# Performance work log

Hardware: AMD Instinct MI355X
Metric: run time of the kernel (lower is better)

The kernel has to match this reference:

```python
import jax, jax.numpy as jnp
import numpy as np


def _hard_sigmoid(x):
    # Keras ConvLSTM2D default recurrent_activation
    return jnp.clip(0.2 * x + 0.5, 0.0, 1.0)


def _conv_same(x, w):
    # x: [B,H,W,Cin], w: [kh,kw,Cin,Cout]
    return jax.lax.conv_general_dilated(
        x, w, window_strides=(1, 1), padding='SAME',
        dimension_numbers=('NHWC', 'HWIO', 'NHWC'))


def setup_inputs() -> dict:
    key = jax.random.key(0)
    ks = jax.random.split(key, 6)
    B, T, H, W, F = 16, 16, 64, 64, 64
    return {
        'inputs': jax.random.normal(ks[0], (B, T, H, W, 1), jnp.float32),  # only T is used
        'h0': jax.random.normal(ks[1], (B, H, W, F), jnp.float32),
        'c0': jax.random.normal(ks[2], (B, H, W, F), jnp.float32),
        'kernels': jax.random.normal(ks[3], (T, 3, 3, F, 4 * F), jnp.float32) * 0.05,
        'rec_kernels': jax.random.normal(ks[4], (T, 3, 3, F, 4 * F), jnp.float32) * 0.05,
        'bias': jnp.zeros((T, 4 * F), jnp.float32),
    }


def reference(inputs, h0, c0, kernels, rec_kernels, bias):
    # The layer feeds h back as the cell input each step, so the cell input x == h.
    # By linearity, conv(h, Wk) + conv(h, Uk) == conv(h, Wk + Uk); we fuse the two convs.
    # Gate order (Keras ConvLSTM2DCell): i, f, c, o.
    def step(carry, params):
        h, c = carry
        Wk, Uk, b = params  # [3,3,F,4F], [3,3,F,4F], [4F]
        z = _conv_same(h, Wk + Uk) + b  # [B,H,W,4F]
        zi, zf, zc, zo = jnp.split(z, 4, axis=-1)
        i = _hard_sigmoid(zi)
        f = _hard_sigmoid(zf)
        c_new = f * c + i * jnp.tanh(zc)
        o = _hard_sigmoid(zo)
        h_new = o * jnp.tanh(c_new)
        return (h_new, c_new), h_new

    (_, _), hs = jax.lax.scan(step, (h0, c0), (kernels, rec_kernels, bias))
    return jnp.moveaxis(hs, 0, 1)  # [B, T, H, W, F]
```

## Files before the change

### kernel.cpp

```cpp
#include <hip/hip_runtime.h>
#include <math.h>

typedef _Float16 f16;
typedef _Float16 f16x4 __attribute__((ext_vector_type(4)));
typedef _Float16 f16x8 __attribute__((ext_vector_type(8)));
typedef float f32x4 __attribute__((ext_vector_type(4)));

#define NB 16
#define NT 16
#define NH 64
#define NW 64
#define NF 64
#define NG 256
#define HWF ((size_t)NH * NW * NF)
#define OUT_BSTRIDE ((size_t)NT * HWF)
#define RS2 8448
#define WSTEP ((size_t)18432)

#define MFMA(a, b, c) __builtin_amdgcn_mfma_f32_16x16x32_f16((a), (b), (c), 0, 0, 0)

__device__ __forceinline__ void gload_lds16(const void* g, void* l) {
    __builtin_amdgcn_global_load_lds(
        (const __attribute__((address_space(1))) unsigned int*)(g),
        (__attribute__((address_space(3))) unsigned int*)(l), 16, 0, 0);
}

__device__ __forceinline__ float hsig(float x) {
    return fminf(fmaxf(0.2f * x + 0.5f, 0.0f), 1.0f);
}

__device__ __forceinline__ float ftanh(float x) {
    float t = __builtin_amdgcn_exp2f(x * 2.885390081777927f);
    return 1.0f - 2.0f * __builtin_amdgcn_rcpf(t + 1.0f);
}

__global__ void fuse_w_hi(const float* __restrict__ k, const float* __restrict__ rk,
                          f16* __restrict__ wf2) {
    int idx = blockIdx.x * 256 + threadIdx.x;
    if (idx >= NT * 9 * NG * 8) return;
    int g8   = idx & 7;
    int cout = (idx >> 3) & 255;
    int tt   = idx >> 11;
    int tap  = tt % 9;
    int t    = tt / 9;
    int kk = g8 >> 2, lg = g8 & 3;

    const float* ks = k  + (size_t)tt * NF * NG + cout;
    const float* rs = rk + (size_t)tt * NF * NG + cout;

    f16 hi8[8];
#pragma unroll
    for (int j = 0; j < 8; ++j) {
        int cin = kk * 32 + lg * 8 + j;
        hi8[j] = (f16)(ks[(size_t)cin * NG] + rs[(size_t)cin * NG]);
    }
    const int lane = lg * 16 + (cout & 15);
    const int cb   = ((cout >> 4) & 3) * 4 + (cout >> 6);
    size_t chunk = (size_t)t * WSTEP + (size_t)(tap * 2 + kk) * 1024 +
                   (size_t)cb * 64 + lane;
    *(f16x8*)&wf2[chunk * 8] = *(f16x8*)hi8;
}

__global__ void f32_to_f16(const float* __restrict__ src, f16* __restrict__ dst, int n4) {
    int i = blockIdx.x * 256 + threadIdx.x;
    if (i >= n4) return;
    float4 v = ((const float4*)src)[i];
    f16x4 o = { (f16)v.x, (f16)v.y, (f16)v.z, (f16)v.w };
    *(f16x4*)&dst[(size_t)i * 4] = o;
}

__global__ void __launch_bounds__(512, 2)
convlstm_mfma_step(const f16* __restrict__ h2in, f16* __restrict__ h2out,
                   f16* __restrict__ cbuf,
                   float* __restrict__ hout,
                   const f16* __restrict__ wt,
                   const float* __restrict__ bias)
{
    __shared__ __align__(16) unsigned char lds[6 * RS2];

    const int tid  = threadIdx.x;
    const int w    = tid >> 6;
    const int lane = tid & 63;

    const int id = blockIdx.x;
    const int bb = ((id & 7) << 1) + ((id >> 7) & 1);
    const int y0 = ((id >> 3) & 15) * 4;

    const int wm = w >> 2;
    const int wn = w & 3;
    const int lm = lane & 15;
    const int lg = lane >> 4;

    const f16x8* wb = (const f16x8*)wt + (size_t)(wn * 4) * 64 + lane;
    f16x8 bh[4];
#pragma unroll
    for (int nf = 0; nf < 4; ++nf)
        bh[nf] = wb[nf * 64];

    const int f = wn * 16 + lm;
    f16 cp[8][4];
#pragma unroll
    for (int mf = 0; mf < 8; ++mf) {
        const int gy = y0 + wm * 2 + (mf >> 2);
        const int xb = (mf & 3) * 16 + lg * 4;
        const size_t base = ((((size_t)bb * NH + gy) * NW + xb) << 6) + f;
#pragma unroll
        for (int j = 0; j < 4; ++j)
            cp[mf][j] = cbuf[base + (size_t)j * 64];
    }

    if (tid < 96) {
        int row = tid >> 4, side = (tid >> 3) & 1, j = tid & 7;
        *(f16x8*)&lds[row * RS2 + side * (65 * 128) + j * 16] = (f16x8)(_Float16)0.0f;
    }

    {
        const int x = w * 8 + (lane >> 3);
        const int g = lane & 7;
        const unsigned src = ((unsigned)x << 7) +
                             ((unsigned)(g ^ ((x + 1) & 7)) << 4);
#pragma unroll
        for (int k = 0; k < 6; ++k) {
            const int gy = y0 - 1 + k;
            const unsigned dbase = k * RS2 + 128 + w * 1024;
            if (gy >= 0 && gy < NH) {
                const unsigned char* gsrc = (const unsigned char*)h2in +
                    ((((size_t)bb * NH + gy) * NW) << 7);
                gload_lds16(gsrc + src, (void*)&lds[dbase]);
            } else {
                *(f16x8*)&lds[dbase + lane * 16] = (f16x8)(_Float16)0.0f;
            }
        }
    }
    __syncthreads();

    f32x4 acc[8][4];
#pragma unroll
    for (int mf = 0; mf < 8; ++mf)
#pragma unroll
        for (int nf = 0; nf < 4; ++nf) acc[mf][nf] = (f32x4)0.0f;

    unsigned av[3][2];
#pragma unroll
    for (int d = 0; d < 3; ++d)
#pragma unroll
        for (int kk = 0; kk < 2; ++kk) {
            const int tx = lm + d;
            av[d][kk] = (unsigned)(tx * 128 +
                        (((kk * 4 + lg) ^ (tx & 7)) << 4));
        }

#pragma unroll
    for (int it = 0; it < 18; ++it) {
        if (it > 0) {
#pragma unroll
            for (int nf = 0; nf < 4; ++nf)
                bh[nf] = wb[(size_t)it * 1024 + nf * 64];
        }
        const int tap = it >> 1, kk = it & 1;
        const int ty = tap / 3;
        const int d  = tap - ty * 3;
        const unsigned abase = (unsigned)((wm * 2 + ty) * RS2) + av[d][kk];
        __builtin_amdgcn_s_setprio(1);
#pragma unroll
        for (int mf = 0; mf < 8; ++mf) {
            const f16x8 ah = *(const f16x8*)&lds[abase + (mf >> 2) * RS2 +
                                                 (mf & 3) * 2048];
#pragma unroll
            for (int nf = 0; nf < 4; ++nf)
                acc[mf][nf] = MFMA(ah, bh[nf], acc[mf][nf]);
        }
        __builtin_amdgcn_s_setprio(0);
    }

    const float b0 = bias[f], b1 = bias[64 + f], b2 = bias[128 + f], b3 = bias[192 + f];

#pragma unroll
    for (int mf = 0; mf < 8; ++mf) {
        const int gy = y0 + wm * 2 + (mf >> 2);
        const int xb = (mf & 3) * 16 + lg * 4;
        const size_t base = ((((size_t)bb * NH + gy) * NW + xb) << 6) + f;
#pragma unroll
        for (int j = 0; j < 4; ++j) {
            const float zi  = acc[mf][0][j] + b0;
            const float zfv = acc[mf][1][j] + b1;
            const float zc  = acc[mf][2][j] + b2;
            const float zo  = acc[mf][3][j] + b3;
            const float ig = hsig(zi), fg = hsig(zfv), og = hsig(zo);
            const float cn = fg * (float)cp[mf][j] + ig * ftanh(zc);
            cbuf[base + (size_t)j * 64] = (f16)cn;
            const float hn = og * ftanh(cn);
            hout[(size_t)bb * OUT_BSTRIDE + (((size_t)gy * NW + xb + j) << 6) + f] = hn;
            h2out[base + (size_t)j * 64] = (f16)hn;
        }
    }
}

extern "C" void kernel_launch(void* const* d_in, const int* in_sizes, int n_in,
                              void* d_out, int out_size, void* d_ws, size_t ws_size,
                              hipStream_t stream) {
    const float* h0    = (const float*)d_in[1];
    const float* c0    = (const float*)d_in[2];
    const float* kern  = (const float*)d_in[3];
    const float* rkern = (const float*)d_in[4];
    const float* bias  = (const float*)d_in[5];
    float* out = (float*)d_out;

    f16* wf2   = (f16*)d_ws;
    f16* h2a   = wf2 + (size_t)NT * WSTEP * 8;
    f16* h2b   = h2a + (size_t)NB * HWF;
    f16* cbuf  = h2b + (size_t)NB * HWF;

    const int n4 = (int)(NB * HWF / 4);
    fuse_w_hi<<<(NT * 9 * NG * 8 + 255) / 256, 256, 0, stream>>>(kern, rkern, wf2);
    f32_to_f16<<<(n4 + 255) / 256, 256, 0, stream>>>(h0, h2a, n4);
    f32_to_f16<<<(n4 + 255) / 256, 256, 0, stream>>>(c0, cbuf, n4);

    for (int t = 0; t < NT; ++t) {
        const f16* hin = (t & 1) ? h2b : h2a;
        f16* hnx       = (t & 1) ? h2a : h2b;
        convlstm_mfma_step<<<dim3(256), 512, 0, stream>>>(
            hin, hnx, cbuf,
            out + (size_t)t * HWF,
            wf2 + (size_t)t * WSTEP * 8,
            bias + t * NG);
    }
}
```

Before: 378.8 us.

## Fuse timestep launches into persistent cooperative kernel with neighbor flag sync

Replaces the 16 per-timestep launches with one cooperative persistent kernel. Each block keeps its h tile in LDS and its cell state in fp32 registers across steps, and exchanges only the halo rows with neighbouring y-blocks through global edge buffers and per-step flags. The aim is to remove launch overhead and the full reload of h and c every step. The cost is spin-wait synchronisation, system-scope stores and loads, and dependence on cooperative launch succeeding; the old multi-launch path stays as a fallback. The setprio hints are also dropped and the per-iteration weight load is moved up.

```diff
diff --git a/kernel.cpp b/kernel.cpp
--- a/kernel.cpp
+++ b/kernel.cpp
@@ -2,7 +2,7 @@
 #include <math.h>
 
 typedef _Float16 f16;
-typedef _Float16 f16x4 __attribute__((ext_vector_type(4)));
+typedef _Float16 f16x4v __attribute__((ext_vector_type(4)));
 typedef _Float16 f16x8 __attribute__((ext_vector_type(8)));
 typedef float f32x4 __attribute__((ext_vector_type(4)));
 
@@ -16,6 +16,7 @@
 #define OUT_BSTRIDE ((size_t)NT * HWF)
 #define RS2 8448
 #define WSTEP ((size_t)18432)
+#define FSTR 16
 
 #define MFMA(a, b, c) __builtin_amdgcn_mfma_f32_16x16x32_f16((a), (b), (c), 0, 0, 0)
 
@@ -65,16 +66,22 @@
     int i = blockIdx.x * 256 + threadIdx.x;
     if (i >= n4) return;
     float4 v = ((const float4*)src)[i];
-    f16x4 o = { (f16)v.x, (f16)v.y, (f16)v.z, (f16)v.w };
-    *(f16x4*)&dst[(size_t)i * 4] = o;
+    f16x4v o = { (f16)v.x, (f16)v.y, (f16)v.z, (f16)v.w };
+    *(f16x4v*)&dst[(size_t)i * 4] = o;
+}
+
+__global__ void zero_flags(int* __restrict__ flags) {
+    flags[blockIdx.x * 256 + threadIdx.x] = 0;
 }
 
 __global__ void __launch_bounds__(512, 2)
-convlstm_mfma_step(const f16* __restrict__ h2in, f16* __restrict__ h2out,
-                   f16* __restrict__ cbuf,
-                   float* __restrict__ hout,
-                   const f16* __restrict__ wt,
-                   const float* __restrict__ bias)
+convlstm_persist(const f16* __restrict__ wf2,
+                 const f16* __restrict__ h2init,
+                 f16* __restrict__ e0, f16* __restrict__ e1,
+                 const float* __restrict__ c0,
+                 float* __restrict__ out,
+                 const float* __restrict__ bias_all,
+                 int* __restrict__ flags)
 {
     __shared__ __align__(16) unsigned char lds[6 * RS2];
 
@@ -84,36 +91,209 @@
 
     const int id = blockIdx.x;
     const int bb = ((id & 7) << 1) + ((id >> 7) & 1);
-    const int y0 = ((id >> 3) & 15) * 4;
-
-    const int wm = w >> 2;
-    const int wn = w & 3;
-    const int lm = lane & 15;
-    const int lg = lane >> 4;
-
-    const f16x8* wb = (const f16x8*)wt + (size_t)(wn * 4) * 64 + lane;
-    f16x8 bh[4];
-#pragma unroll
-    for (int nf = 0; nf < 4; ++nf)
-        bh[nf] = wb[nf * 64];
-
-    const int f = wn * 16 + lm;
-    f16 cp[8][4];
+    const int iy = (id >> 3) & 15;
+    const int y0 = iy * 4;
+
+    const int wm = w >> 2, wn = w & 3, lm = lane & 15, lg = lane >> 4;
+    const int f  = wn * 16 + lm;
+
+    if (tid < 96) {
+        int row = tid >> 4, side = (tid >> 3) & 1, j = tid & 7;
+        *(f16x8*)&lds[row * RS2 + side * (65 * 128) + j * 16] = (f16x8)(_Float16)0.0f;
+    }
+    {
+        const int x = w * 8 + (lane >> 3);
+        const int g = lane & 7;
+        const unsigned src = ((unsigned)x << 7) +
+                             ((unsigned)(g ^ ((x + 1) & 7)) << 4);
+#pragma unroll
+        for (int k = 0; k < 6; ++k) {
+            const int gy = y0 - 1 + k;
+            const unsigned dbase = k * RS2 + 128 + w * 1024;
+            if (gy >= 0 && gy < NH) {
+                const unsigned char* gsrc = (const unsigned char*)h2init +
+                    ((((size_t)bb * NH + gy) * NW) << 7);
+                gload_lds16(gsrc + src, (void*)&lds[dbase]);
+            } else {
+                *(f16x8*)&lds[dbase + lane * 16] = (f16x8)(_Float16)0.0f;
+            }
+        }
+    }
+
+    float cp[8][4];
 #pragma unroll
     for (int mf = 0; mf < 8; ++mf) {
         const int gy = y0 + wm * 2 + (mf >> 2);
         const int xb = (mf & 3) * 16 + lg * 4;
         const size_t base = ((((size_t)bb * NH + gy) * NW + xb) << 6) + f;
 #pragma unroll
-        for (int j = 0; j < 4; ++j)
-            cp[mf][j] = cbuf[base + (size_t)j * 64];
+        for (int j = 0; j < 4; ++j) cp[mf][j] = c0[base + (size_t)j * 64];
+    }
+
+    unsigned av[3][2];
+#pragma unroll
+    for (int d = 0; d < 3; ++d)
+#pragma unroll
+        for (int kk = 0; kk < 2; ++kk) {
+            const int tx = lm + d;
+            av[d][kk] = (unsigned)(tx * 128 + (((kk * 4 + lg) ^ (tx & 7)) << 4));
+        }
+
+    __syncthreads();
+
+#pragma unroll 1
+    for (int t = 0; t < NT; ++t) {
+        const f16x8* wb = (const f16x8*)(wf2 + (size_t)t * WSTEP * 8) +
+                          (size_t)(wn * 4) * 64 + lane;
+        const float* bias = bias_all + t * NG;
+
+        f32x4 acc[8][4];
+#pragma unroll
+        for (int mf = 0; mf < 8; ++mf)
+#pragma unroll
+            for (int nf = 0; nf < 4; ++nf) acc[mf][nf] = (f32x4)0.0f;
+
+        f16x8 bh[4];
+#pragma unroll
+        for (int it = 0; it < 18; ++it) {
+#pragma unroll
+            for (int nf = 0; nf < 4; ++nf)
+                bh[nf] = wb[(size_t)it * 1024 + nf * 64];
+            const int tap = it >> 1, kk = it & 1;
+            const int ty = tap / 3;
+            const int d  = tap - ty * 3;
+            const unsigned abase = (unsigned)((wm * 2 + ty) * RS2) + av[d][kk];
+#pragma unroll
+            for (int mf = 0; mf < 8; ++mf) {
+                const f16x8 ah = *(const f16x8*)&lds[abase + (mf >> 2) * RS2 +
+                                                     (mf & 3) * 2048];
+#pragma unroll
+                for (int nf = 0; nf < 4; ++nf)
+                    acc[mf][nf] = MFMA(ah, bh[nf], acc[mf][nf]);
+            }
+        }
+
+        __syncthreads();
+
+        const float b0 = bias[f], b1 = bias[64 + f], b2 = bias[128 + f], b3 = bias[192 + f];
+        f16* eW = (t & 1) ? e1 : e0;
+        const bool last = (t == NT - 1);
+
+#pragma unroll
+        for (int mf = 0; mf < 8; ++mf) {
+            const int gy = y0 + wm * 2 + (mf >> 2);
+            const int xb = (mf & 3) * 16 + lg * 4;
+            const bool isEdge = (wm == 0) ? (mf < 4) : (mf >= 4);
+#pragma unroll
+            for (int j = 0; j < 4; ++j) {
+                const float zi  = acc[mf][0][j] + b0;
+                const float zfv = acc[mf][1][j] + b1;
+                const float zc  = acc[mf][2][j] + b2;
+                const float zo  = acc[mf][3][j] + b3;
+                const float ig = hsig(zi), fg = hsig(zfv), og = hsig(zo);
+                const float cn = fg * cp[mf][j] + ig * ftanh(zc);
+                cp[mf][j] = cn;
+                const float hn = og * ftanh(cn);
+                out[(size_t)bb * OUT_BSTRIDE + (size_t)t * HWF +
+                    (((size_t)gy * NW + xb + j) << 6) + f] = hn;
+                if (!last) {
+                    f16 hv = (f16)hn;
+                    const int x = xb + j;
+                    const unsigned loff = (unsigned)((wm * 2 + (mf >> 2) + 1) * RS2 +
+                        128 + x * 128 + (((f >> 3) ^ ((x + 1) & 7)) << 4) + (f & 7) * 2);
+                    *(f16*)&lds[loff] = hv;
+                    if (isEdge) {
+                        const f16* ep = eW + ((((size_t)bb * NH + gy) * NW + x) << 6) + f;
+                        int hb = (int)*(unsigned short*)&hv;
+                        asm volatile("global_store_short %0, %1, off sc0 sc1"
+                                     :: "v"(ep), "v"(hb) : "memory");
+                    }
+                }
+            }
+        }
+
+        if (!last) {
+            __syncthreads();
+
+            if (tid == 0) {
+                const int fbase = ((t * NB + bb) * 16) * FSTR;
+                __hip_atomic_store(&flags[fbase + iy * FSTR], 1,
+                                   __ATOMIC_RELAXED, __HIP_MEMORY_SCOPE_SYSTEM);
+                if (iy > 0)
+                    while (__hip_atomic_load(&flags[fbase + (iy - 1) * FSTR],
+                           __ATOMIC_RELAXED, __HIP_MEMORY_SCOPE_SYSTEM) == 0)
+                        __builtin_amdgcn_s_sleep(1);
+                if (iy < 15)
+                    while (__hip_atomic_load(&flags[fbase + (iy + 1) * FSTR],
+                           __ATOMIC_RELAXED, __HIP_MEMORY_SCOPE_SYSTEM) == 0)
+                        __builtin_amdgcn_s_sleep(1);
+            }
+            __syncthreads();
+
+            const int gi0 = tid * 2;
+            const int r   = gi0 >> 9;
+            const bool valid = r ? (iy < 15) : (iy > 0);
+            if (valid) {
+                const int gy = r ? (y0 + 4) : (y0 - 1);
+                const int rem0 = gi0 & 511, rem1 = rem0 + 1;
+                const int x0 = rem0 >> 3, g0 = rem0 & 7;
+                const int x1 = rem1 >> 3, g1 = rem1 & 7;
+                const f16* sp0 = eW + ((((size_t)bb * NH + gy) * NW + x0) << 6) + g0 * 8;
+                const f16* sp1 = eW + ((((size_t)bb * NH + gy) * NW + x1) << 6) + g1 * 8;
+                f16x8 v0, v1;
+                asm volatile("global_load_dwordx4 %0, %1, off sc0 sc1"
+                             : "=v"(v0) : "v"(sp0) : "memory");
+                asm volatile("global_load_dwordx4 %0, %1, off sc0 sc1"
+                             : "=v"(v1) : "v"(sp1) : "memory");
+                asm volatile("s_waitcnt vmcnt(0)" ::: "memory");
+                const unsigned slot = (r ? 5u : 0u) * RS2 + 128;
+                unsigned d0 = (unsigned)(uintptr_t)&lds[slot + x0 * 128 +
+                                                        ((g0 ^ ((x0 + 1) & 7)) << 4)];
+                unsigned d1 = (unsigned)(uintptr_t)&lds[slot + x1 * 128 +
+                                                        ((g1 ^ ((x1 + 1) & 7)) << 4)];
+                asm volatile("ds_write_b128 %0, %1" :: "v"(d0), "v"(v0) : "memory");
+                asm volatile("ds_write_b128 %0, %1" :: "v"(d1), "v"(v1) : "memory");
+            }
+            __syncthreads();
+        }
+    }
+}
+
+__global__ void __launch_bounds__(512, 2)
+convlstm_mfma_step(const f16* __restrict__ h2in, f16* __restrict__ h2out,
+                   f16* __restrict__ cbuf, float* __restrict__ hout,
+                   const f16* __restrict__ wt, const float* __restrict__ bias)
+{
+    __shared__ __align__(16) unsigned char lds[6 * RS2];
+
+    const int tid  = threadIdx.x;
+    const int w    = tid >> 6;
+    const int lane = tid & 63;
+    const int id = blockIdx.x;
+    const int bb = ((id & 7) << 1) + ((id >> 7) & 1);
+    const int y0 = ((id >> 3) & 15) * 4;
+    const int wm = w >> 2, wn = w & 3, lm = lane & 15, lg = lane >> 4;
+
+    const f16x8* wb = (const f16x8*)wt + (size_t)(wn * 4) * 64 + lane;
+    f16x8 bh[4];
+#pragma unroll
+    for (int nf = 0; nf < 4; ++nf) bh[nf] = wb[nf * 64];
+
+    const int f = wn * 16 + lm;
+    f16 cp[8][4];
+#pragma unroll
+    for (int mf = 0; mf < 8; ++mf) {
+        const int gy = y0 + wm * 2 + (mf >> 2);
+        const int xb = (mf & 3) * 16 + lg * 4;
+        const size_t base = ((((size_t)bb * NH + gy) * NW + xb) << 6) + f;
+#pragma unroll
+        for (int j = 0; j < 4; ++j) cp[mf][j] = cbuf[base + (size_t)j * 64];
     }
 
     if (tid < 96) {
         int row = tid >> 4, side = (tid >> 3) & 1, j = tid & 7;
         *(f16x8*)&lds[row * RS2 + side * (65 * 128) + j * 16] = (f16x8)(_Float16)0.0f;
     }
-
     {
         const int x = w * 8 + (lane >> 3);
         const int g = lane & 7;
@@ -146,8 +326,7 @@
 #pragma unroll
         for (int kk = 0; kk < 2; ++kk) {
             const int tx = lm + d;
-            av[d][kk] = (unsigned)(tx * 128 +
-                        (((kk * 4 + lg) ^ (tx & 7)) << 4));
+            av[d][kk] = (unsigned)(tx * 128 + (((kk * 4 + lg) ^ (tx & 7)) << 4));
         }
 
 #pragma unroll
@@ -161,7 +340,6 @@
         const int ty = tap / 3;
         const int d  = tap - ty * 3;
         const unsigned abase = (unsigned)((wm * 2 + ty) * RS2) + av[d][kk];
-        __builtin_amdgcn_s_setprio(1);
 #pragma unroll
         for (int mf = 0; mf < 8; ++mf) {
             const f16x8 ah = *(const f16x8*)&lds[abase + (mf >> 2) * RS2 +
@@ -170,11 +348,9 @@
             for (int nf = 0; nf < 4; ++nf)
                 acc[mf][nf] = MFMA(ah, bh[nf], acc[mf][nf]);
         }
-        __builtin_amdgcn_s_setprio(0);
     }
 
     const float b0 = bias[f], b1 = bias[64 + f], b2 = bias[128 + f], b3 = bias[192 + f];
-
 #pragma unroll
     for (int mf = 0; mf < 8; ++mf) {
         const int gy = y0 + wm * 2 + (mf >> 2);
@@ -209,20 +385,35 @@
     f16* wf2   = (f16*)d_ws;
     f16* h2a   = wf2 + (size_t)NT * WSTEP * 8;
     f16* h2b   = h2a + (size_t)NB * HWF;
-    f16* cbuf  = h2b + (size_t)NB * HWF;
+    f16* e1    = h2b + (size_t)NB * HWF;
+    f16* cbuf  = e1  + (size_t)NB * HWF;
+    int* flags = (int*)(cbuf + (size_t)NB * HWF);
 
     const int n4 = (int)(NB * HWF / 4);
     fuse_w_hi<<<(NT * 9 * NG * 8 + 255) / 256, 256, 0, stream>>>(kern, rkern, wf2);
     f32_to_f16<<<(n4 + 255) / 256, 256, 0, stream>>>(h0, h2a, n4);
     f32_to_f16<<<(n4 + 255) / 256, 256, 0, stream>>>(c0, cbuf, n4);
-
-    for (int t = 0; t < NT; ++t) {
-        const f16* hin = (t & 1) ? h2b : h2a;
-        f16* hnx       = (t & 1) ? h2a : h2b;
-        convlstm_mfma_step<<<dim3(256), 512, 0, stream>>>(
-            hin, hnx, cbuf,
-            out + (size_t)t * HWF,
-            wf2 + (size_t)t * WSTEP * 8,
-            bias + t * NG);
-    }
-}
+    zero_flags<<<256, 256, 0, stream>>>(flags);
+
+    const f16* wf2c = wf2;
+    const f16* h2ac = h2a;
+    const float* c0c = c0;
+    const float* biasc = bias;
+    void* args[] = { (void*)&wf2c, (void*)&h2ac, (void*)&h2b, (void*)&e1,
+                     (void*)&c0c, (void*)&out, (void*)&biasc, (void*)&flags };
+    hipError_t ce = hipLaunchCooperativeKernel(
+        (const void*)convlstm_persist, dim3(256), dim3(512), args, 0u, stream);
+
+    if (ce != hipSuccess) {
+        (void)hipGetLastError();
+        for (int t = 0; t < NT; ++t) {
+            const f16* hin = (t & 1) ? h2b : h2a;
+            f16* hnx       = (t & 1) ? h2a : h2b;
+            convlstm_mfma_step<<<dim3(256), 512, 0, stream>>>(
+                hin, hnx, cbuf,
+                out + (size_t)t * HWF,
+                wf2 + (size_t)t * WSTEP * 8,
+                bias + t * NG);
+        }
+    }
+}
```

Result: slower. 627.8 us (+65.8%).

## Reuse LDS A-fragments across vertical taps and prefetch weight fragments

Applied to the files above, without the earlier changes.

Reorders the 18 tap/k-chunk iterations so that, for each (d, kk), the three vertical taps ty=0..2 run back to back. LDS rows loaded for one tap are reused by the next, so each rotating register set is read once instead of twice. Weight fragments for the next tap are loaded into a second register bank before the current MFMAs issue, so global latency overlaps compute. The extra A and B register sets raise VGPR pressure under the 512x2 launch bounds, which risks spills or lower occupancy.

```diff
diff --git a/kernel.cpp b/kernel.cpp
--- a/kernel.cpp
+++ b/kernel.cpp
@@ -2,7 +2,7 @@
 #include <math.h>
 
 typedef _Float16 f16;
-typedef _Float16 f16x4 __attribute__((ext_vector_type(4)));
+typedef _Float16 f16x4v __attribute__((ext_vector_type(4)));
 typedef _Float16 f16x8 __attribute__((ext_vector_type(8)));
 typedef float f32x4 __attribute__((ext_vector_type(4)));
 
@@ -65,8 +65,8 @@
     int i = blockIdx.x * 256 + threadIdx.x;
     if (i >= n4) return;
     float4 v = ((const float4*)src)[i];
-    f16x4 o = { (f16)v.x, (f16)v.y, (f16)v.z, (f16)v.w };
-    *(f16x4*)&dst[(size_t)i * 4] = o;
+    f16x4v o = { (f16)v.x, (f16)v.y, (f16)v.z, (f16)v.w };
+    *(f16x4v*)&dst[(size_t)i * 4] = o;
 }
 
 __global__ void __launch_bounds__(512, 2)
@@ -92,10 +92,6 @@
     const int lg = lane >> 4;
 
     const f16x8* wb = (const f16x8*)wt + (size_t)(wn * 4) * 64 + lane;
-    f16x8 bh[4];
-#pragma unroll
-    for (int nf = 0; nf < 4; ++nf)
-        bh[nf] = wb[nf * 64];
 
     const int f = wn * 16 + lm;
     f16 cp[8][4];
@@ -150,27 +146,74 @@
                         (((kk * 4 + lg) ^ (tx & 7)) << 4));
         }
 
-#pragma unroll
-    for (int it = 0; it < 18; ++it) {
-        if (it > 0) {
+    f16x8 A0[4], A1[4], A2[4], bh0[4], bh1[4];
+
+#pragma unroll
+    for (int kk = 0; kk < 2; ++kk)
+#pragma unroll
+    for (int d = 0; d < 3; ++d) {
+        const unsigned abase = (unsigned)(wm * 2 * RS2) + av[d][kk];
+
+        {
+            const int it0 = d * 2 + kk;
 #pragma unroll
             for (int nf = 0; nf < 4; ++nf)
-                bh[nf] = wb[(size_t)it * 1024 + nf * 64];
-        }
-        const int tap = it >> 1, kk = it & 1;
-        const int ty = tap / 3;
-        const int d  = tap - ty * 3;
-        const unsigned abase = (unsigned)((wm * 2 + ty) * RS2) + av[d][kk];
-        __builtin_amdgcn_s_setprio(1);
-#pragma unroll
-        for (int mf = 0; mf < 8; ++mf) {
-            const f16x8 ah = *(const f16x8*)&lds[abase + (mf >> 2) * RS2 +
-                                                 (mf & 3) * 2048];
+                bh0[nf] = wb[(size_t)it0 * 1024 + nf * 64];
+        }
+#pragma unroll
+        for (int xb = 0; xb < 4; ++xb)
+            A0[xb] = *(const f16x8*)&lds[abase + xb * 2048];
+#pragma unroll
+        for (int xb = 0; xb < 4; ++xb)
+            A1[xb] = *(const f16x8*)&lds[abase + RS2 + xb * 2048];
+
+        {
+            const int it1 = (3 + d) * 2 + kk;
 #pragma unroll
             for (int nf = 0; nf < 4; ++nf)
-                acc[mf][nf] = MFMA(ah, bh[nf], acc[mf][nf]);
-        }
-        __builtin_amdgcn_s_setprio(0);
+                bh1[nf] = wb[(size_t)it1 * 1024 + nf * 64];
+#pragma unroll
+            for (int xb = 0; xb < 4; ++xb)
+                A2[xb] = *(const f16x8*)&lds[abase + 2 * RS2 + xb * 2048];
+            __builtin_amdgcn_s_setprio(1);
+#pragma unroll
+            for (int mf = 0; mf < 8; ++mf) {
+                const f16x8 ah = (mf >> 2) ? A1[mf & 3] : A0[mf & 3];
+#pragma unroll
+                for (int nf = 0; nf < 4; ++nf)
+                    acc[mf][nf] = MFMA(ah, bh0[nf], acc[mf][nf]);
+            }
+            __builtin_amdgcn_s_setprio(0);
+        }
+        {
+            const int it2 = (6 + d) * 2 + kk;
+#pragma unroll
+            for (int nf = 0; nf < 4; ++nf)
+                bh0[nf] = wb[(size_t)it2 * 1024 + nf * 64];
+#pragma unroll
+            for (int xb = 0; xb < 4; ++xb)
+                A0[xb] = *(const f16x8*)&lds[abase + 3 * RS2 + xb * 2048];
+            __builtin_amdgcn_s_setprio(1);
+#pragma unroll
+            for (int mf = 0; mf < 8; ++mf) {
+                const f16x8 ah = (mf >> 2) ? A2[mf & 3] : A1[mf & 3];
+#pragma unroll
+                for (int nf = 0; nf < 4; ++nf)
+                    acc[mf][nf] = MFMA(ah, bh1[nf], acc[mf][nf]);
+            }
+            __builtin_amdgcn_s_setprio(0);
+        }
+        {
+            __builtin_amdgcn_s_setprio(1);
+#pragma unroll
+            for (int mf = 0; mf < 8; ++mf) {
+                const f16x8 ah = (mf >> 2) ? A0[mf & 3] : A2[mf & 3];
+#pragma unroll
+                for (int nf = 0; nf < 4; ++nf)
+                    acc[mf][nf] = MFMA(ah, bh0[nf], acc[mf][nf]);
+            }
+            __builtin_amdgcn_s_setprio(0);
+        }
     }
 
     const float b0 = bias[f], b1 = bias[64 + f], b2 = bias[128 + f], b3 = bias[192 + f];
```

Result: slower. 532.2 us (+40.5%).

## Merge prologue kernels, transpose cell-state layout, skip final-step state stores

Applied to the files above, without the earlier changes.

Folds the weight fusion and the two fp32-to-fp16 conversions into one prologue launch. It also stores the cell state in an [B,H,F,W] layout, so each thread loads and stores four contiguous x values as one vector instead of four scalar strided accesses. The last timestep skips writing c and the fp16 h buffer, which no later step reads. This removes two launches and some scattered memory traffic, but the prologue's c0 transpose now does strided scalar reads.

```diff
diff --git a/kernel.cpp b/kernel.cpp
--- a/kernel.cpp
+++ b/kernel.cpp
@@ -2,7 +2,7 @@
 #include <math.h>
 
 typedef _Float16 f16;
-typedef _Float16 f16x4 __attribute__((ext_vector_type(4)));
+typedef _Float16 f16x4v __attribute__((ext_vector_type(4)));
 typedef _Float16 f16x8 __attribute__((ext_vector_type(8)));
 typedef float f32x4 __attribute__((ext_vector_type(4)));
 
@@ -34,39 +34,51 @@
     return 1.0f - 2.0f * __builtin_amdgcn_rcpf(t + 1.0f);
 }
 
-__global__ void fuse_w_hi(const float* __restrict__ k, const float* __restrict__ rk,
-                          f16* __restrict__ wf2) {
-    int idx = blockIdx.x * 256 + threadIdx.x;
-    if (idx >= NT * 9 * NG * 8) return;
-    int g8   = idx & 7;
-    int cout = (idx >> 3) & 255;
-    int tt   = idx >> 11;
-    int tap  = tt % 9;
-    int t    = tt / 9;
-    int kk = g8 >> 2, lg = g8 & 3;
-
-    const float* ks = k  + (size_t)tt * NF * NG + cout;
-    const float* rs = rk + (size_t)tt * NF * NG + cout;
-
-    f16 hi8[8];
-#pragma unroll
-    for (int j = 0; j < 8; ++j) {
-        int cin = kk * 32 + lg * 8 + j;
-        hi8[j] = (f16)(ks[(size_t)cin * NG] + rs[(size_t)cin * NG]);
-    }
-    const int lane = lg * 16 + (cout & 15);
-    const int cb   = ((cout >> 4) & 3) * 4 + (cout >> 6);
-    size_t chunk = (size_t)t * WSTEP + (size_t)(tap * 2 + kk) * 1024 +
-                   (size_t)cb * 64 + lane;
-    *(f16x8*)&wf2[chunk * 8] = *(f16x8*)hi8;
-}
-
-__global__ void f32_to_f16(const float* __restrict__ src, f16* __restrict__ dst, int n4) {
-    int i = blockIdx.x * 256 + threadIdx.x;
-    if (i >= n4) return;
-    float4 v = ((const float4*)src)[i];
-    f16x4 o = { (f16)v.x, (f16)v.y, (f16)v.z, (f16)v.w };
-    *(f16x4*)&dst[(size_t)i * 4] = o;
+__global__ void prologue_all(const float* __restrict__ k, const float* __restrict__ rk,
+                             f16* __restrict__ wf2,
+                             const float* __restrict__ h0, f16* __restrict__ h2,
+                             const float* __restrict__ c0, f16* __restrict__ cbuf) {
+    const int blk = blockIdx.x;
+    const int tid = threadIdx.x;
+
+    if (blk < 1152) {
+        int idx = blk * 256 + tid;
+        int g8   = idx & 7;
+        int cout = (idx >> 3) & 255;
+        int tt   = idx >> 11;
+        int tap  = tt % 9;
+        int t    = tt / 9;
+        int kk = g8 >> 2, lg = g8 & 3;
+
+        const float* ks = k  + (size_t)tt * NF * NG + cout;
+        const float* rs = rk + (size_t)tt * NF * NG + cout;
+
+        f16 hi8[8];
+#pragma unroll
+        for (int j = 0; j < 8; ++j) {
+            int cin = kk * 32 + lg * 8 + j;
+            hi8[j] = (f16)(ks[(size_t)cin * NG] + rs[(size_t)cin * NG]);
+        }
+        const int lane = lg * 16 + (cout & 15);
+        const int cb   = ((cout >> 4) & 3) * 4 + (cout >> 6);
+        size_t chunk = (size_t)t * WSTEP + (size_t)(tap * 2 + kk) * 1024 +
+                       (size_t)cb * 64 + lane;
+        *(f16x8*)&wf2[chunk * 8] = *(f16x8*)hi8;
+    } else if (blk < 5248) {
+        int i = (blk - 1152) * 256 + tid;
+        float4 v = ((const float4*)h0)[i];
+        f16x4v o = { (f16)v.x, (f16)v.y, (f16)v.z, (f16)v.w };
+        *(f16x4v*)&h2[(size_t)i * 4] = o;
+    } else {
+        int i = (blk - 5248) * 256 + tid;
+        int bgy = i >> 10;
+        int rem = i & 1023;
+        int x4  = rem >> 6;
+        int f   = rem & 63;
+        const float* src = c0 + (size_t)bgy * 4096 + (size_t)x4 * 256 + f;
+        f16x4v o = { (f16)src[0], (f16)src[64], (f16)src[128], (f16)src[192] };
+        *(f16x4v*)&cbuf[((size_t)bgy * 64 + f) * 64 + x4 * 4] = o;
+    }
 }
 
 __global__ void __launch_bounds__(512, 2)
@@ -74,7 +86,8 @@
                    f16* __restrict__ cbuf,
                    float* __restrict__ hout,
                    const f16* __restrict__ wt,
-                   const float* __restrict__ bias)
+                   const float* __restrict__ bias,
+                   int last)
 {
     __shared__ __align__(16) unsigned char lds[6 * RS2];
 
@@ -92,21 +105,19 @@
     const int lg = lane >> 4;
 
     const f16x8* wb = (const f16x8*)wt + (size_t)(wn * 4) * 64 + lane;
+
     f16x8 bh[4];
 #pragma unroll
     for (int nf = 0; nf < 4; ++nf)
         bh[nf] = wb[nf * 64];
 
     const int f = wn * 16 + lm;
-    f16 cp[8][4];
+    f16x4v cp[8];
 #pragma unroll
     for (int mf = 0; mf < 8; ++mf) {
         const int gy = y0 + wm * 2 + (mf >> 2);
         const int xb = (mf & 3) * 16 + lg * 4;
-        const size_t base = ((((size_t)bb * NH + gy) * NW + xb) << 6) + f;
-#pragma unroll
-        for (int j = 0; j < 4; ++j)
-            cp[mf][j] = cbuf[base + (size_t)j * 64];
+        cp[mf] = *(const f16x4v*)&cbuf[(((size_t)bb * NH + gy) * NF + f) * 64 + xb];
     }
 
     if (tid < 96) {
@@ -120,9 +131,9 @@
         const unsigned src = ((unsigned)x << 7) +
                              ((unsigned)(g ^ ((x + 1) & 7)) << 4);
 #pragma unroll
-        for (int k = 0; k < 6; ++k) {
-            const int gy = y0 - 1 + k;
-            const unsigned dbase = k * RS2 + 128 + w * 1024;
+        for (int kr = 0; kr < 6; ++kr) {
+            const int gy = y0 - 1 + kr;
+            const unsigned dbase = kr * RS2 + 128 + w * 1024;
             if (gy >= 0 && gy < NH) {
                 const unsigned char* gsrc = (const unsigned char*)h2in +
                     ((((size_t)bb * NH + gy) * NW) << 7);
@@ -179,7 +190,8 @@
     for (int mf = 0; mf < 8; ++mf) {
         const int gy = y0 + wm * 2 + (mf >> 2);
         const int xb = (mf & 3) * 16 + lg * 4;
-        const size_t base = ((((size_t)bb * NH + gy) * NW + xb) << 6) + f;
+        const size_t hbase = ((((size_t)bb * NH + gy) * NW + xb) << 6) + f;
+        f16x4v cn4, hn4;
 #pragma unroll
         for (int j = 0; j < 4; ++j) {
             const float zi  = acc[mf][0][j] + b0;
@@ -188,10 +200,16 @@
             const float zo  = acc[mf][3][j] + b3;
             const float ig = hsig(zi), fg = hsig(zfv), og = hsig(zo);
             const float cn = fg * (float)cp[mf][j] + ig * ftanh(zc);
-            cbuf[base + (size_t)j * 64] = (f16)cn;
+            cn4[j] = (f16)cn;
             const float hn = og * ftanh(cn);
+            hn4[j] = (f16)hn;
             hout[(size_t)bb * OUT_BSTRIDE + (((size_t)gy * NW + xb + j) << 6) + f] = hn;
-            h2out[base + (size_t)j * 64] = (f16)hn;
+        }
+        if (!last) {
+            *(f16x4v*)&cbuf[(((size_t)bb * NH + gy) * NF + f) * 64 + xb] = cn4;
+#pragma unroll
+            for (int j = 0; j < 4; ++j)
+                h2out[hbase + (size_t)j * 64] = hn4[j];
         }
     }
 }
@@ -211,10 +229,7 @@
     f16* h2b   = h2a + (size_t)NB * HWF;
     f16* cbuf  = h2b + (size_t)NB * HWF;
 
-    const int n4 = (int)(NB * HWF / 4);
-    fuse_w_hi<<<(NT * 9 * NG * 8 + 255) / 256, 256, 0, stream>>>(kern, rkern, wf2);
-    f32_to_f16<<<(n4 + 255) / 256, 256, 0, stream>>>(h0, h2a, n4);
-    f32_to_f16<<<(n4 + 255) / 256, 256, 0, stream>>>(c0, cbuf, n4);
+    prologue_all<<<dim3(9344), 256, 0, stream>>>(kern, rkern, wf2, h0, h2a, c0, cbuf);
 
     for (int t = 0; t < NT; ++t) {
         const f16* hin = (t & 1) ? h2b : h2a;
@@ -223,6 +238,7 @@
             hin, hnx, cbuf,
             out + (size_t)t * HWF,
             wf2 + (size_t)t * WSTEP * 8,
-            bias + t * NG);
-    }
-}
+            bias + t * NG,
+            (t == NT - 1) ? 1 : 0);
+    }
+}
```

New measurement: 380.6 us. Within noise of the previous version (+0.5%).
